# Performance work log

Measured on AMD Instinct MI355X. Metric: run time of the kernel, lower is better.

Reference implementation:

```python
import jax, jax.numpy as jnp
from jax import lax
import numpy as np

B, N, C = 128, 196, 768
H = 8
HD = C // H  # 96
FF = 3       # focusing factor
KS = 5       # dwc kernel size


def setup_inputs() -> dict:
    key = jax.random.key(0)
    ks = jax.random.split(key, 12)
    std = 0.02
    inp = {
        'x': jax.random.normal(ks[0], (B, N, C), dtype=jnp.float32),
        'Wq': jax.random.normal(ks[1], (C, C), dtype=jnp.float32) * std,
        'bq': jnp.zeros((C,), dtype=jnp.float32),
        'Wk': jax.random.normal(ks[2], (C, C), dtype=jnp.float32) * std,
        'bk': jnp.zeros((C,), dtype=jnp.float32),
        'Wv': jax.random.normal(ks[3], (C, C), dtype=jnp.float32) * std,
        'bv': jnp.zeros((C,), dtype=jnp.float32),
        'pos_enc': jax.random.normal(ks[4], (1, N, C), dtype=jnp.float32) * std,
        'scale_param': jnp.zeros((1, 1, C), dtype=jnp.float32),
        'dwc_w': jax.random.normal(ks[5], (HD, 1, KS, KS), dtype=jnp.float32) * np.sqrt(2.0 / (KS * KS)),
        'dwc_b': jnp.zeros((HD,), dtype=jnp.float32),
        'Wp': jax.random.normal(ks[6], (C, C), dtype=jnp.float32) * std,
        'bp': jnp.zeros((C,), dtype=jnp.float32),
    }
    return inp


def _focused_attn(x, Wq, bq, Wk, bk, Wv, bv, pos_enc, scale_param, dwc_w, dwc_b, Wp, bp):
    b, n, c = x.shape
    q = x @ Wq + bq
    k = x @ Wk + bk
    v = x @ Wv + bv
    k = k + pos_enc

    scale = jax.nn.softplus(scale_param)
    q = (jax.nn.relu(q) + 1e-6) / scale
    k = (jax.nn.relu(k) + 1e-6) / scale
    # focusing: raise to power FF, restore original L2 norm (over full channel dim)
    q_norm = jnp.linalg.norm(q, axis=-1, keepdims=True)
    k_norm = jnp.linalg.norm(k, axis=-1, keepdims=True)
    q = q ** FF
    k = k ** FF
    q = q / jnp.linalg.norm(q, axis=-1, keepdims=True) * q_norm
    k = k / jnp.linalg.norm(k, axis=-1, keepdims=True) * k_norm

    # (b, n, H*hd) -> (b*H, n, hd)
    def split_heads(t):
        return t.reshape(b, n, H, HD).transpose(0, 2, 1, 3).reshape(b * H, n, HD)

    q, k, v = split_heads(q), split_heads(k), split_heads(v)

    i = j = n
    cdim = ddim = HD
    z = 1.0 / (jnp.einsum('bic,bc->bi', q, k.sum(axis=1)) + 1e-6)
    if i * j * (cdim + ddim) > cdim * ddim * (i + j):
        kv = jnp.einsum('bjc,bjd->bcd', k, v)              # (b*H, hd, hd)
        out = jnp.einsum('bic,bcd,bi->bid', q, kv, z)
    else:
        qk = jnp.einsum('bic,bjc->bij', q, k)
        out = jnp.einsum('bij,bjd,bi->bid', qk, v, z)

    # depthwise conv feature map on v reshaped to sqrt(n) x sqrt(n)
    num = int(round(n ** 0.5))
    fm = v.transpose(0, 2, 1).reshape(b * H, HD, num, num)
    fm = lax.conv_general_dilated(
        fm, dwc_w, window_strides=(1, 1), padding='SAME',
        feature_group_count=HD,
        dimension_numbers=('NCHW', 'OIHW', 'NCHW'))
    fm = fm + dwc_b[None, :, None, None]
    fm = fm.reshape(b * H, HD, n).transpose(0, 2, 1)

    out = out + fm
    out = out.reshape(b, H, n, HD).transpose(0, 2, 1, 3).reshape(b, n, c)
    return out @ Wp + bp


def reference(x, Wq, bq, Wk, bk, Wv, bv, pos_enc, scale_param, dwc_w, dwc_b, Wp, bp):
    return _focused_attn(x, Wq, bq, Wk, bk, Wv, bv, pos_enc, scale_param, dwc_w, dwc_b, Wp, bp)
```

## Files before the change

kernel.cpp:

```cpp
#include <hip/hip_runtime.h>
#include <hip/hip_bf16.h>
#include <math.h>


#define MROWS 25088
#define CDIM 768
#define HDIM 96
#define NTOK 196
#define BHN 1024
#define K2 1536
#define LDP 40

typedef __attribute__((ext_vector_type(8))) short bf16x8;
typedef __attribute__((ext_vector_type(4))) float f32x4;

__device__ __forceinline__ short f2bf(float x) {
  unsigned u = __float_as_uint(x);
  unsigned r = (u + 0x7fffu + ((u >> 16) & 1u)) >> 16;
  return (short)r;
}
__device__ __forceinline__ float bf2f(short s) {
  return __uint_as_float(((unsigned)(unsigned short)s) << 16);
}

__global__ __launch_bounds__(256) void split_wt(const float* __restrict__ W0,
                                                const float* __restrict__ W1,
                                                const float* __restrict__ W2,
                                                const float* __restrict__ W3,
                                                short* __restrict__ outbase) {
  const float* W;
  switch (blockIdx.z) {
    case 0: W = W0; break;
    case 1: W = W1; break;
    case 2: W = W2; break;
    default: W = W3; break;
  }
  short* O = outbase + (size_t)blockIdx.z * 768 * K2;
  __shared__ float t[32][33];
  const int n0 = blockIdx.x * 32, k0 = blockIdx.y * 32;
  const int tx = threadIdx.x & 31, ty = threadIdx.x >> 5;
#pragma unroll
  for (int i = 0; i < 32; i += 8) t[ty + i][tx] = W[(size_t)(k0 + ty + i) * 768 + n0 + tx];
  __syncthreads();
#pragma unroll
  for (int i = 0; i < 32; i += 8) {
    float v = t[tx][ty + i];
    short h = f2bf(v), l = f2bf(v - bf2f(h));
    O[(size_t)(n0 + ty + i) * K2 + k0 + tx] = h;
    O[(size_t)(n0 + ty + i) * K2 + 768 + k0 + tx] = l;
  }
}

__device__ __forceinline__ void gemm_mfma_body(const float* __restrict__ A,
                                               const short* __restrict__ Bt2,
                                               const float* __restrict__ bias,
                                               const float* __restrict__ pos,
                                               float* __restrict__ C, bool addPos) {
  __shared__ short Ah[128 * LDP];
  __shared__ short Al[128 * LDP];
  __shared__ short Bh[128 * LDP];
  __shared__ short Bl[128 * LDP];
  const int tid = threadIdx.x;
  const int lane = tid & 63;
  const int w = tid >> 6, wr = w >> 1, wc = w & 1;
  const int row0 = blockIdx.y * 128, col0 = blockIdx.x * 128;

  const int srow = tid >> 1;
  const int scol = (tid & 1) << 4;
  const float* gA = A + (size_t)(row0 + srow) * CDIM + scol;
  const short* gBh = Bt2 + (size_t)(col0 + srow) * K2 + scol;
  short* lAh = Ah + srow * LDP + scol;
  short* lAl = Al + srow * LDP + scol;
  short* lBh = Bh + srow * LDP + scol;
  short* lBl = Bl + srow * LDP + scol;

  f32x4 acc[4][4];
#pragma unroll
  for (int i = 0; i < 4; i++)
#pragma unroll
    for (int j = 0; j < 4; j++) acc[i][j] = (f32x4){0.f, 0.f, 0.f, 0.f};

  const int fr = lane & 15;
  const int kg = (lane >> 4) << 3;

#pragma unroll 1
  for (int k0 = 0; k0 < CDIM; k0 += 32) {
    float av[16];
    *(float4*)&av[0]  = *(const float4*)(gA + k0);
    *(float4*)&av[4]  = *(const float4*)(gA + k0 + 4);
    *(float4*)&av[8]  = *(const float4*)(gA + k0 + 8);
    *(float4*)&av[12] = *(const float4*)(gA + k0 + 12);
    bf16x8 bh0 = *(const bf16x8*)(gBh + k0);
    bf16x8 bh1 = *(const bf16x8*)(gBh + k0 + 8);
    bf16x8 bl0 = *(const bf16x8*)(gBh + 768 + k0);
    bf16x8 bl1 = *(const bf16x8*)(gBh + 768 + k0 + 8);

    bf16x8 ahv[2], alv[2];
#pragma unroll
    for (int i = 0; i < 16; i++) {
      short hh = f2bf(av[i]);
      short ll = f2bf(av[i] - bf2f(hh));
      ahv[i >> 3][i & 7] = hh;
      alv[i >> 3][i & 7] = ll;
    }

    __syncthreads();
    *(bf16x8*)(lAh) = ahv[0]; *(bf16x8*)(lAh + 8) = ahv[1];
    *(bf16x8*)(lAl) = alv[0]; *(bf16x8*)(lAl + 8) = alv[1];
    *(bf16x8*)(lBh) = bh0;    *(bf16x8*)(lBh + 8) = bh1;
    *(bf16x8*)(lBl) = bl0;    *(bf16x8*)(lBl + 8) = bl1;
    __syncthreads();

    bf16x8 fah[4], fal[4], fbh[4], fbl[4];
#pragma unroll
    for (int i = 0; i < 4; i++) {
      const int ar = (wr * 64 + i * 16 + fr) * LDP + kg;
      const int br = (wc * 64 + i * 16 + fr) * LDP + kg;
      fah[i] = *(const bf16x8*)&Ah[ar];
      fal[i] = *(const bf16x8*)&Al[ar];
      fbh[i] = *(const bf16x8*)&Bh[br];
      fbl[i] = *(const bf16x8*)&Bl[br];
    }
#pragma unroll
    for (int i = 0; i < 4; i++)
#pragma unroll
      for (int j = 0; j < 4; j++)
        acc[i][j] = __builtin_amdgcn_mfma_f32_16x16x32_bf16(fah[i], fbh[j], acc[i][j], 0, 0, 0);
#pragma unroll
    for (int i = 0; i < 4; i++)
#pragma unroll
      for (int j = 0; j < 4; j++)
        acc[i][j] = __builtin_amdgcn_mfma_f32_16x16x32_bf16(fah[i], fbl[j], acc[i][j], 0, 0, 0);
#pragma unroll
    for (int i = 0; i < 4; i++)
#pragma unroll
      for (int j = 0; j < 4; j++)
        acc[i][j] = __builtin_amdgcn_mfma_f32_16x16x32_bf16(fal[i], fbh[j], acc[i][j], 0, 0, 0);
  }

  const int rg = (lane >> 4) * 4;
#pragma unroll
  for (int i = 0; i < 4; i++) {
#pragma unroll
    for (int j = 0; j < 4; j++) {
      f32x4 v = acc[i][j];
      const int gcol = col0 + wc * 64 + j * 16 + fr;
      const float bb = bias[gcol];
#pragma unroll
      for (int r = 0; r < 4; r++) {
        const int grow = row0 + wr * 64 + i * 16 + rg + r;
        float val = v[r] + bb;
        if (addPos) val += pos[(grow % NTOK) * CDIM + gcol];
        C[(size_t)grow * CDIM + gcol] = val;
      }
    }
  }
}

__global__ __launch_bounds__(256) void mfma_qkv(const float* __restrict__ x,
    const short* __restrict__ wt2,
    const float* __restrict__ b0, const float* __restrict__ b1, const float* __restrict__ b2,
    const float* __restrict__ pos,
    float* __restrict__ o0, float* __restrict__ o1, float* __restrict__ o2) {
  const short* Bt; const float* bias; float* C; bool addPos = false;
  switch (blockIdx.z) {
    case 0: Bt = wt2;                        bias = b0; C = o0; break;
    case 1: Bt = wt2 + (size_t)768 * K2;     bias = b1; C = o1; addPos = true; break;
    default: Bt = wt2 + (size_t)2 * 768 * K2; bias = b2; C = o2; break;
  }
  gemm_mfma_body(x, Bt, bias, pos, C, addPos);
}

__global__ __launch_bounds__(256) void mfma_proj(const float* __restrict__ y,
    const short* __restrict__ wt2p, const float* __restrict__ bias,
    float* __restrict__ C) {
  gemm_mfma_body(y, wt2p, bias, nullptr, C, false);
}

__device__ __forceinline__ void block_reduce2(float& a, float& b, float* sbuf, int tid) {
#pragma unroll
  for (int off = 32; off > 0; off >>= 1) {
    a += __shfl_down(a, off, 64);
    b += __shfl_down(b, off, 64);
  }
  __syncthreads();
  if ((tid & 63) == 0) {
    int w = tid >> 6;
    sbuf[w] = a;
    sbuf[4 + w] = b;
  }
  __syncthreads();
  a = sbuf[0] + sbuf[1] + sbuf[2] + sbuf[3];
  b = sbuf[4] + sbuf[5] + sbuf[6] + sbuf[7];
}

__global__ __launch_bounds__(256) void focus_kernel(float* __restrict__ q,
                                                    float* __restrict__ k,
                                                    const float* __restrict__ sp) {
  const int row = blockIdx.x;
  const int tid = threadIdx.x;
  __shared__ float sbuf[8];
  float* qb = q + (size_t)row * CDIM;
  float* kb = k + (size_t)row * CDIM;

  float tq[3], tk[3];
  float sq = 0.f, sk = 0.f;
#pragma unroll
  for (int s = 0; s < 3; s++) {
    int c = tid + s * 256;
    float scp = sp[c];
    float scale = fmaxf(scp, 0.f) + log1pf(expf(-fabsf(scp)));
    float aq = (fmaxf(qb[c], 0.f) + 1e-6f) / scale;
    float ak = (fmaxf(kb[c], 0.f) + 1e-6f) / scale;
    tq[s] = aq; tk[s] = ak;
    sq += aq * aq; sk += ak * ak;
  }
  block_reduce2(sq, sk, sbuf, tid);
  float nq1 = sqrtf(sq), nk1 = sqrtf(sk);

  float uq[3], uk[3];
  float s2q = 0.f, s2k = 0.f;
#pragma unroll
  for (int s = 0; s < 3; s++) {
    uq[s] = tq[s] * tq[s] * tq[s];
    uk[s] = tk[s] * tk[s] * tk[s];
    s2q += uq[s] * uq[s];
    s2k += uk[s] * uk[s];
  }
  block_reduce2(s2q, s2k, sbuf, tid);
  float rq = nq1 / sqrtf(s2q);
  float rk = nk1 / sqrtf(s2k);
#pragma unroll
  for (int s = 0; s < 3; s++) {
    int c = tid + s * 256;
    qb[c] = uq[s] * rq;
    kb[c] = uk[s] * rk;
  }
}

__global__ __launch_bounds__(128) void ksum_kernel(const float* __restrict__ k,
                                                   float* __restrict__ ksum) {
  const int bh = blockIdx.x;
  const int b = bh >> 3, h = bh & 7;
  const int d = threadIdx.x;
  if (d >= HDIM) return;
  const float* base = k + (size_t)(b * NTOK) * CDIM + h * HDIM + d;
  float s = 0.f;
  for (int j = 0; j < NTOK; ++j) s += base[(size_t)j * CDIM];
  ksum[bh * HDIM + d] = s;
}

__global__ __launch_bounds__(256) void kv_kernel(const float* __restrict__ k,
                                                 const float* __restrict__ v,
                                                 float* __restrict__ kv) {
  const int bh = blockIdx.x;
  const int b = bh >> 3, h = bh & 7;
  const size_t base = (size_t)(b * NTOK) * CDIM + h * HDIM;
  __shared__ float ks[28][96];
  __shared__ float vs[28][96];
  const int tid = threadIdx.x;
  const int tx = tid & 15, ty = tid >> 4;
  float acc[6][6];
#pragma unroll
  for (int i = 0; i < 6; i++)
#pragma unroll
    for (int j = 0; j < 6; j++) acc[i][j] = 0.f;

  for (int j0 = 0; j0 < NTOK; j0 += 28) {
    for (int idx = tid; idx < 28 * 96; idx += 256) {
      int jr = idx / 96, d = idx % 96;
      size_t g = base + (size_t)(j0 + jr) * CDIM + d;
      ks[jr][d] = k[g];
      vs[jr][d] = v[g];
    }
    __syncthreads();
#pragma unroll 4
    for (int j = 0; j < 28; ++j) {
      float a[6], bb[6];
#pragma unroll
      for (int i = 0; i < 6; i++) a[i] = ks[j][ty * 6 + i];
#pragma unroll
      for (int i = 0; i < 6; i++) bb[i] = vs[j][tx * 6 + i];
#pragma unroll
      for (int i = 0; i < 6; i++)
#pragma unroll
        for (int jj = 0; jj < 6; jj++) acc[i][jj] += a[i] * bb[jj];
    }
    __syncthreads();
  }
#pragma unroll
  for (int i = 0; i < 6; i++)
#pragma unroll
    for (int j = 0; j < 6; j++)
      kv[(size_t)bh * (HDIM * HDIM) + (ty * 6 + i) * HDIM + tx * 6 + j] = acc[i][j];
}

__global__ __launch_bounds__(256) void attn_out_kernel(const float* __restrict__ q,
                                                       const float* __restrict__ kvmat,
                                                       const float* __restrict__ ksum,
                                                       float* __restrict__ y) {
  const int bh = blockIdx.x;
  const int b = bh >> 3, h = bh & 7;
  const size_t base = (size_t)(b * NTOK) * CDIM + h * HDIM;
  __shared__ float kvs[HDIM * HDIM];
  __shared__ float qs[64][97];
  __shared__ float ksum_s[HDIM];
  const int tid = threadIdx.x;
  const int tx = tid & 15, ty = tid >> 4;
  const int d0 = tx * 6;

  for (int idx = tid; idx < HDIM * HDIM; idx += 256) kvs[idx] = kvmat[(size_t)bh * (HDIM * HDIM) + idx];
  if (tid < HDIM) ksum_s[tid] = ksum[bh * HDIM + tid];

  for (int i0 = 0; i0 < NTOK; i0 += 64) {
    int nrows = NTOK - i0; if (nrows > 64) nrows = 64;
    __syncthreads();
    for (int idx = tid; idx < nrows * 96; idx += 256) {
      int rr = idx / 96, d = idx % 96;
      qs[rr][d] = q[base + (size_t)(i0 + rr) * CDIM + d];
    }
    __syncthreads();

    float zz[4];
#pragma unroll
    for (int rr = 0; rr < 4; rr++) {
      int r = ty * 4 + rr;
      float part = 0.f;
#pragma unroll
      for (int i = 0; i < 6; i++) part += qs[r][d0 + i] * ksum_s[d0 + i];
#pragma unroll
      for (int m = 8; m >= 1; m >>= 1) part += __shfl_xor(part, m, 16);
      zz[rr] = 1.f / (part + 1e-6f);
    }

    float acc[4][6];
#pragma unroll
    for (int rr = 0; rr < 4; rr++)
#pragma unroll
      for (int i = 0; i < 6; i++) acc[rr][i] = 0.f;

    for (int c = 0; c < HDIM; ++c) {
      float kvv[6];
#pragma unroll
      for (int i = 0; i < 6; i++) kvv[i] = kvs[c * HDIM + d0 + i];
#pragma unroll
      for (int rr = 0; rr < 4; rr++) {
        float qv = qs[ty * 4 + rr][c];
#pragma unroll
        for (int i = 0; i < 6; i++) acc[rr][i] += qv * kvv[i];
      }
    }
#pragma unroll
    for (int rr = 0; rr < 4; rr++) {
      int r = i0 + ty * 4 + rr;
      if (r < NTOK) {
#pragma unroll
        for (int i = 0; i < 6; i++) y[base + (size_t)r * CDIM + d0 + i] = acc[rr][i] * zz[rr];
      }
    }
  }
}

__global__ __launch_bounds__(256) void dwconv_kernel(const float* __restrict__ v,
                                                     const float* __restrict__ w,
                                                     const float* __restrict__ bias,
                                                     float* __restrict__ y) {
  const int bh = blockIdx.x;
  const int b = bh >> 3, h = bh & 7;
  const int ch0 = blockIdx.y * 32;
  const size_t base = (size_t)(b * NTOK) * CDIM + h * HDIM + ch0;
  __shared__ float vs[NTOK][32];
  __shared__ float ws_s[32][25];
  const int tid = threadIdx.x;

  for (int idx = tid; idx < NTOK * 32; idx += 256) {
    int j = idx >> 5, ch = idx & 31;
    vs[j][ch] = v[base + (size_t)j * CDIM + ch];
  }
  for (int idx = tid; idx < 32 * 25; idx += 256) {
    int ch = idx / 25, kk = idx % 25;
    ws_s[ch][kk] = w[(ch0 + ch) * 25 + kk];
  }
  __syncthreads();

  const int ch = tid & 31, pg = tid >> 5;
  const float bval = bias[ch0 + ch];
  for (int p = pg; p < NTOK; p += 8) {
    int r = p / 14, cl = p % 14;
    float acc = 0.f;
#pragma unroll
    for (int dr = 0; dr < 5; dr++) {
      int rr = r + dr - 2;
      if (rr < 0 || rr >= 14) continue;
#pragma unroll
      for (int dc = 0; dc < 5; dc++) {
        int cc = cl + dc - 2;
        if (cc < 0 || cc >= 14) continue;
        acc += vs[rr * 14 + cc][ch] * ws_s[ch][dr * 5 + dc];
      }
    }
    y[base + (size_t)p * CDIM + ch] += acc + bval;
  }
}

extern "C" void kernel_launch(void* const* d_in, const int* in_sizes, int n_in,
                              void* d_out, int out_size, void* d_ws, size_t ws_size,
                              hipStream_t stream) {
  const float* x    = (const float*)d_in[0];
  const float* Wq   = (const float*)d_in[1];
  const float* bq   = (const float*)d_in[2];
  const float* Wk   = (const float*)d_in[3];
  const float* bk   = (const float*)d_in[4];
  const float* Wv   = (const float*)d_in[5];
  const float* bv   = (const float*)d_in[6];
  const float* pos  = (const float*)d_in[7];
  const float* sp   = (const float*)d_in[8];
  const float* dwcw = (const float*)d_in[9];
  const float* dwcb = (const float*)d_in[10];
  const float* Wp   = (const float*)d_in[11];
  const float* bp   = (const float*)d_in[12];
  float* out = (float*)d_out;

  const size_t MC = (size_t)MROWS * CDIM;
  char* ws = (char*)d_ws;
  float* k    = (float*)(ws);
  float* v    = (float*)(ws + MC * 4);
  short* wt2  = (short*)(ws + 2 * MC * 4);
  float* kv   = (float*)(ws + 2 * MC * 4 + (size_t)4 * 768 * K2 * 2);
  float* ksum = kv + (size_t)BHN * HDIM * HDIM;
  float* q = out;
  float* y = k;

  split_wt<<<dim3(24, 24, 4), 256, 0, stream>>>(Wq, Wk, Wv, Wp, wt2);
  mfma_qkv<<<dim3(6, 196, 3), 256, 0, stream>>>(x, wt2, bq, bk, bv, pos, q, k, v);
  focus_kernel<<<MROWS, 256, 0, stream>>>(q, k, sp);
  ksum_kernel<<<BHN, 128, 0, stream>>>(k, ksum);
  kv_kernel<<<BHN, 256, 0, stream>>>(k, v, kv);
  attn_out_kernel<<<BHN, 256, 0, stream>>>(q, kv, ksum, y);
  dwconv_kernel<<<dim3(BHN, 3), 256, 0, stream>>>(v, dwcw, dwcb, y);
  mfma_proj<<<dim3(6, 196, 1), 256, 0, stream>>>(y, wt2 + (size_t)3 * 768 * K2, bp, out);
}
```

Before: 1.010 ms.

## Use direct global-to-LDS loads with swizzle, tile remap, and wave-per-row focus

The GEMM body now loads the pre-split bf16 weight tiles straight into LDS with global_load_lds. It replaces the padded LDS layout with an XOR-swizzled unpadded one to avoid bank conflicts, remaps block indices for locality, and uses packed bf16x2 conversion for the activation hi/lo split. The focus kernel now processes one row per wavefront with float4 accesses and shuffle-only reductions, which removes block-level syncs and quarters the launch count. These changes aim to cut LDS traffic, register pressure and sync overhead, but the swizzle and tile remap must exactly match the fragment reads.

```diff
diff --git a/kernel.cpp b/kernel.cpp
--- a/kernel.cpp
+++ b/kernel.cpp
@@ -9,7 +9,6 @@
 #define NTOK 196
 #define BHN 1024
 #define K2 1536
-#define LDP 40
 
 typedef __attribute__((ext_vector_type(8))) short bf16x8;
 typedef __attribute__((ext_vector_type(4))) float f32x4;
@@ -21,6 +20,27 @@
 }
 __device__ __forceinline__ float bf2f(short s) {
   return __uint_as_float(((unsigned)(unsigned short)s) << 16);
+}
+
+__device__ __forceinline__ void gload16(const short* g, short* l) {
+  __builtin_amdgcn_global_load_lds(
+      (const __attribute__((address_space(1))) void*)g,
+      (__attribute__((address_space(3))) void*)l, 16, 0, 0);
+}
+
+__device__ __forceinline__ unsigned cvt2(float x, float y, float& rx, float& ry) {
+  __hip_bfloat162 hb = __float22bfloat162_rn(make_float2(x, y));
+  float2 hf = __bfloat1622float2(hb);
+  rx = x - hf.x; ry = y - hf.y;
+  unsigned u;
+  __builtin_memcpy(&u, &hb, 4);
+  return u;
+}
+__device__ __forceinline__ unsigned cvt2n(float x, float y) {
+  __hip_bfloat162 hb = __float22bfloat162_rn(make_float2(x, y));
+  unsigned u;
+  __builtin_memcpy(&u, &hb, 4);
+  return u;
 }
 
 __global__ __launch_bounds__(256) void split_wt(const float* __restrict__ W0,
@@ -56,23 +76,37 @@
                                                const float* __restrict__ bias,
                                                const float* __restrict__ pos,
                                                float* __restrict__ C, bool addPos) {
-  __shared__ short Ah[128 * LDP];
-  __shared__ short Al[128 * LDP];
-  __shared__ short Bh[128 * LDP];
-  __shared__ short Bl[128 * LDP];
+  __shared__ short Ah[128 * 32];
+  __shared__ short Al[128 * 32];
+  __shared__ short Bh[128 * 32];
+  __shared__ short Bl[128 * 32];
   const int tid = threadIdx.x;
   const int lane = tid & 63;
   const int w = tid >> 6, wr = w >> 1, wc = w & 1;
-  const int row0 = blockIdx.y * 128, col0 = blockIdx.x * 128;
-
-  const int srow = tid >> 1;
-  const int scol = (tid & 1) << 4;
-  const float* gA = A + (size_t)(row0 + srow) * CDIM + scol;
-  const short* gBh = Bt2 + (size_t)(col0 + srow) * K2 + scol;
-  short* lAh = Ah + srow * LDP + scol;
-  short* lAl = Al + srow * LDP + scol;
-  short* lBh = Bh + srow * LDP + scol;
-  short* lBl = Bl + srow * LDP + scol;
+
+  const int hw = blockIdx.x + 6 * blockIdx.y;
+  const int tile = (hw & 7) * 147 + (hw >> 3);
+  const int bx = tile % 6, by = tile / 6;
+  const int row0 = by * 128, col0 = bx * 128;
+
+  const int ar = tid >> 1;
+  const int ah_ = tid & 1;
+  const int am = (tid >> 2) & 3;
+  const int s0 = (2 * ah_) ^ am, s1 = (2 * ah_ + 1) ^ am;
+  const float* gA = A + (size_t)(row0 + ar) * CDIM + ah_ * 16;
+  short* lAh0 = Ah + ar * 32 + s0 * 8;
+  short* lAh1 = Ah + ar * 32 + s1 * 8;
+  short* lAl0 = Al + ar * 32 + s0 * 8;
+  short* lAl1 = Al + ar * 32 + s1 * 8;
+
+  const int brow = w * 32 + (lane >> 2);
+  const int bslot = (lane & 3) ^ ((lane >> 3) & 3);
+  const short* gBh = Bt2 + (size_t)(col0 + brow) * K2 + bslot * 8;
+  const short* gBl = gBh + 768;
+  short* ldsBh0 = Bh + (w * 32) * 32;
+  short* ldsBh1 = Bh + (w * 32 + 16) * 32;
+  short* ldsBl0 = Bl + (w * 32) * 32;
+  short* ldsBl1 = Bl + (w * 32 + 16) * 32;
 
   f32x4 acc[4][4];
 #pragma unroll
@@ -81,45 +115,50 @@
     for (int j = 0; j < 4; j++) acc[i][j] = (f32x4){0.f, 0.f, 0.f, 0.f};
 
   const int fr = lane & 15;
-  const int kg = (lane >> 4) << 3;
+  const int k16 = lane >> 4;
+  const int rslot = k16 ^ ((fr >> 1) & 3);
+  const int rofs = fr * 32 + rslot * 8;
 
 #pragma unroll 1
   for (int k0 = 0; k0 < CDIM; k0 += 32) {
-    float av[16];
-    *(float4*)&av[0]  = *(const float4*)(gA + k0);
-    *(float4*)&av[4]  = *(const float4*)(gA + k0 + 4);
-    *(float4*)&av[8]  = *(const float4*)(gA + k0 + 8);
-    *(float4*)&av[12] = *(const float4*)(gA + k0 + 12);
-    bf16x8 bh0 = *(const bf16x8*)(gBh + k0);
-    bf16x8 bh1 = *(const bf16x8*)(gBh + k0 + 8);
-    bf16x8 bl0 = *(const bf16x8*)(gBh + 768 + k0);
-    bf16x8 bl1 = *(const bf16x8*)(gBh + 768 + k0 + 8);
-
-    bf16x8 ahv[2], alv[2];
-#pragma unroll
-    for (int i = 0; i < 16; i++) {
-      short hh = f2bf(av[i]);
-      short ll = f2bf(av[i] - bf2f(hh));
-      ahv[i >> 3][i & 7] = hh;
-      alv[i >> 3][i & 7] = ll;
-    }
-
-    __syncthreads();
-    *(bf16x8*)(lAh) = ahv[0]; *(bf16x8*)(lAh + 8) = ahv[1];
-    *(bf16x8*)(lAl) = alv[0]; *(bf16x8*)(lAl + 8) = alv[1];
-    *(bf16x8*)(lBh) = bh0;    *(bf16x8*)(lBh + 8) = bh1;
-    *(bf16x8*)(lBl) = bl0;    *(bf16x8*)(lBl + 8) = bl1;
+    float4 a0 = *(const float4*)(gA + k0);
+    float4 a1 = *(const float4*)(gA + k0 + 4);
+    float4 a2 = *(const float4*)(gA + k0 + 8);
+    float4 a3 = *(const float4*)(gA + k0 + 12);
+    float r[16];
+    unsigned h0 = cvt2(a0.x, a0.y, r[0], r[1]);
+    unsigned h1 = cvt2(a0.z, a0.w, r[2], r[3]);
+    unsigned h2 = cvt2(a1.x, a1.y, r[4], r[5]);
+    unsigned h3 = cvt2(a1.z, a1.w, r[6], r[7]);
+    unsigned h4 = cvt2(a2.x, a2.y, r[8], r[9]);
+    unsigned h5 = cvt2(a2.z, a2.w, r[10], r[11]);
+    unsigned h6 = cvt2(a3.x, a3.y, r[12], r[13]);
+    unsigned h7 = cvt2(a3.z, a3.w, r[14], r[15]);
+    unsigned l0 = cvt2n(r[0], r[1]),  l1 = cvt2n(r[2], r[3]);
+    unsigned l2 = cvt2n(r[4], r[5]),  l3 = cvt2n(r[6], r[7]);
+    unsigned l4 = cvt2n(r[8], r[9]),  l5 = cvt2n(r[10], r[11]);
+    unsigned l6 = cvt2n(r[12], r[13]), l7 = cvt2n(r[14], r[15]);
+
+    __syncthreads();
+    gload16(gBh + k0, ldsBh0);
+    gload16(gBh + 16 * K2 + k0, ldsBh1);
+    gload16(gBl + k0, ldsBl0);
+    gload16(gBl + 16 * K2 + k0, ldsBl1);
+    *(uint4*)lAh0 = make_uint4(h0, h1, h2, h3);
+    *(uint4*)lAh1 = make_uint4(h4, h5, h6, h7);
+    *(uint4*)lAl0 = make_uint4(l0, l1, l2, l3);
+    *(uint4*)lAl1 = make_uint4(l4, l5, l6, l7);
     __syncthreads();
 
     bf16x8 fah[4], fal[4], fbh[4], fbl[4];
 #pragma unroll
     for (int i = 0; i < 4; i++) {
-      const int ar = (wr * 64 + i * 16 + fr) * LDP + kg;
-      const int br = (wc * 64 + i * 16 + fr) * LDP + kg;
-      fah[i] = *(const bf16x8*)&Ah[ar];
-      fal[i] = *(const bf16x8*)&Al[ar];
-      fbh[i] = *(const bf16x8*)&Bh[br];
-      fbl[i] = *(const bf16x8*)&Bl[br];
+      const int arr = (wr * 64 + i * 16) * 32 + rofs;
+      const int brr = (wc * 64 + i * 16) * 32 + rofs;
+      fah[i] = *(const bf16x8*)&Ah[arr];
+      fal[i] = *(const bf16x8*)&Al[arr];
+      fbh[i] = *(const bf16x8*)&Bh[brr];
+      fbl[i] = *(const bf16x8*)&Bl[brr];
     }
 #pragma unroll
     for (int i = 0; i < 4; i++)
@@ -147,9 +186,9 @@
       const int gcol = col0 + wc * 64 + j * 16 + fr;
       const float bb = bias[gcol];
 #pragma unroll
-      for (int r = 0; r < 4; r++) {
-        const int grow = row0 + wr * 64 + i * 16 + rg + r;
-        float val = v[r] + bb;
+      for (int r2 = 0; r2 < 4; r2++) {
+        const int grow = row0 + wr * 64 + i * 16 + rg + r2;
+        float val = v[r2] + bb;
         if (addPos) val += pos[(grow % NTOK) * CDIM + gcol];
         C[(size_t)grow * CDIM + gcol] = val;
       }
@@ -164,8 +203,8 @@
     float* __restrict__ o0, float* __restrict__ o1, float* __restrict__ o2) {
   const short* Bt; const float* bias; float* C; bool addPos = false;
   switch (blockIdx.z) {
-    case 0: Bt = wt2;                        bias = b0; C = o0; break;
-    case 1: Bt = wt2 + (size_t)768 * K2;     bias = b1; C = o1; addPos = true; break;
+    case 0: Bt = wt2;                         bias = b0; C = o0; break;
+    case 1: Bt = wt2 + (size_t)768 * K2;      bias = b1; C = o1; addPos = true; break;
     default: Bt = wt2 + (size_t)2 * 768 * K2; bias = b2; C = o2; break;
   }
   gemm_mfma_body(x, Bt, bias, pos, C, addPos);
@@ -177,64 +216,72 @@
   gemm_mfma_body(y, wt2p, bias, nullptr, C, false);
 }
 
-__device__ __forceinline__ void block_reduce2(float& a, float& b, float* sbuf, int tid) {
+__device__ __forceinline__ void wave_reduce2(float& a, float& b) {
 #pragma unroll
   for (int off = 32; off > 0; off >>= 1) {
-    a += __shfl_down(a, off, 64);
-    b += __shfl_down(b, off, 64);
-  }
-  __syncthreads();
-  if ((tid & 63) == 0) {
-    int w = tid >> 6;
-    sbuf[w] = a;
-    sbuf[4 + w] = b;
-  }
-  __syncthreads();
-  a = sbuf[0] + sbuf[1] + sbuf[2] + sbuf[3];
-  b = sbuf[4] + sbuf[5] + sbuf[6] + sbuf[7];
+    a += __shfl_xor(a, off, 64);
+    b += __shfl_xor(b, off, 64);
+  }
 }
 
 __global__ __launch_bounds__(256) void focus_kernel(float* __restrict__ q,
                                                     float* __restrict__ k,
                                                     const float* __restrict__ sp) {
-  const int row = blockIdx.x;
-  const int tid = threadIdx.x;
-  __shared__ float sbuf[8];
+  const int row = blockIdx.x * 4 + (threadIdx.x >> 6);
+  const int lane = threadIdx.x & 63;
   float* qb = q + (size_t)row * CDIM;
   float* kb = k + (size_t)row * CDIM;
 
-  float tq[3], tk[3];
+  float tq[12], tk[12];
   float sq = 0.f, sk = 0.f;
 #pragma unroll
   for (int s = 0; s < 3; s++) {
-    int c = tid + s * 256;
-    float scp = sp[c];
-    float scale = fmaxf(scp, 0.f) + log1pf(expf(-fabsf(scp)));
-    float aq = (fmaxf(qb[c], 0.f) + 1e-6f) / scale;
-    float ak = (fmaxf(kb[c], 0.f) + 1e-6f) / scale;
-    tq[s] = aq; tk[s] = ak;
-    sq += aq * aq; sk += ak * ak;
-  }
-  block_reduce2(sq, sk, sbuf, tid);
-  float nq1 = sqrtf(sq), nk1 = sqrtf(sk);
-
-  float uq[3], uk[3];
+    const int c = s * 256 + lane * 4;
+    float4 qv = *(const float4*)&qb[c];
+    float4 kv4 = *(const float4*)&kb[c];
+    float4 spv = *(const float4*)&sp[c];
+#pragma unroll
+    for (int j = 0; j < 4; j++) {
+      float scp = j == 0 ? spv.x : j == 1 ? spv.y : j == 2 ? spv.z : spv.w;
+      float qq  = j == 0 ? qv.x  : j == 1 ? qv.y  : j == 2 ? qv.z  : qv.w;
+      float kk  = j == 0 ? kv4.x : j == 1 ? kv4.y : j == 2 ? kv4.z : kv4.w;
+      float scale = fmaxf(scp, 0.f) + log1pf(expf(-fabsf(scp)));
+      float inv = 1.f / scale;
+      float aq = (fmaxf(qq, 0.f) + 1e-6f) * inv;
+      float ak = (fmaxf(kk, 0.f) + 1e-6f) * inv;
+      tq[s * 4 + j] = aq; tk[s * 4 + j] = ak;
+      sq += aq * aq; sk += ak * ak;
+    }
+  }
+  wave_reduce2(sq, sk);
+  const float nq1 = sqrtf(sq), nk1 = sqrtf(sk);
+
   float s2q = 0.f, s2k = 0.f;
 #pragma unroll
+  for (int j = 0; j < 12; j++) {
+    float cq = tq[j] * tq[j] * tq[j];
+    float ck = tk[j] * tk[j] * tk[j];
+    s2q += cq * cq; s2k += ck * ck;
+  }
+  wave_reduce2(s2q, s2k);
+  const float rq = nq1 / sqrtf(s2q);
+  const float rk = nk1 / sqrtf(s2k);
+
+#pragma unroll
   for (int s = 0; s < 3; s++) {
-    uq[s] = tq[s] * tq[s] * tq[s];
-    uk[s] = tk[s] * tk[s] * tk[s];
-    s2q += uq[s] * uq[s];
-    s2k += uk[s] * uk[s];
-  }
-  block_reduce2(s2q, s2k, sbuf, tid);
-  float rq = nq1 / sqrtf(s2q);
-  float rk = nk1 / sqrtf(s2k);
-#pragma unroll
-  for (int s = 0; s < 3; s++) {
-    int c = tid + s * 256;
-    qb[c] = uq[s] * rq;
-    kb[c] = uk[s] * rk;
+    const int c = s * 256 + lane * 4;
+    float4 oq, ok;
+#pragma unroll
+    for (int j = 0; j < 4; j++) {
+      float a = tq[s * 4 + j], b = tk[s * 4 + j];
+      float vq = a * a * a * rq, vk = b * b * b * rk;
+      if (j == 0) { oq.x = vq; ok.x = vk; }
+      else if (j == 1) { oq.y = vq; ok.y = vk; }
+      else if (j == 2) { oq.z = vq; ok.z = vk; }
+      else { oq.w = vq; ok.w = vk; }
+    }
+    *(float4*)&qb[c] = oq;
+    *(float4*)&kb[c] = ok;
   }
 }
 
@@ -324,10 +371,10 @@
     float zz[4];
 #pragma unroll
     for (int rr = 0; rr < 4; rr++) {
-      int r = ty * 4 + rr;
+      int r2 = ty * 4 + rr;
       float part = 0.f;
 #pragma unroll
-      for (int i = 0; i < 6; i++) part += qs[r][d0 + i] * ksum_s[d0 + i];
+      for (int i = 0; i < 6; i++) part += qs[r2][d0 + i] * ksum_s[d0 + i];
 #pragma unroll
       for (int m = 8; m >= 1; m >>= 1) part += __shfl_xor(part, m, 16);
       zz[rr] = 1.f / (part + 1e-6f);
@@ -352,10 +399,10 @@
     }
 #pragma unroll
     for (int rr = 0; rr < 4; rr++) {
-      int r = i0 + ty * 4 + rr;
-      if (r < NTOK) {
-#pragma unroll
-        for (int i = 0; i < 6; i++) y[base + (size_t)r * CDIM + d0 + i] = acc[rr][i] * zz[rr];
+      int r2 = i0 + ty * 4 + rr;
+      if (r2 < NTOK) {
+#pragma unroll
+        for (int i = 0; i < 6; i++) y[base + (size_t)r2 * CDIM + d0 + i] = acc[rr][i] * zz[rr];
       }
     }
   }
@@ -386,11 +433,11 @@
   const int ch = tid & 31, pg = tid >> 5;
   const float bval = bias[ch0 + ch];
   for (int p = pg; p < NTOK; p += 8) {
-    int r = p / 14, cl = p % 14;
+    int r2 = p / 14, cl = p % 14;
     float acc = 0.f;
 #pragma unroll
     for (int dr = 0; dr < 5; dr++) {
-      int rr = r + dr - 2;
+      int rr = r2 + dr - 2;
       if (rr < 0 || rr >= 14) continue;
 #pragma unroll
       for (int dc = 0; dc < 5; dc++) {
@@ -433,7 +480,7 @@
 
   split_wt<<<dim3(24, 24, 4), 256, 0, stream>>>(Wq, Wk, Wv, Wp, wt2);
   mfma_qkv<<<dim3(6, 196, 3), 256, 0, stream>>>(x, wt2, bq, bk, bv, pos, q, k, v);
-  focus_kernel<<<MROWS, 256, 0, stream>>>(q, k, sp);
+  focus_kernel<<<MROWS / 4, 256, 0, stream>>>(q, k, sp);
   ksum_kernel<<<BHN, 128, 0, stream>>>(k, ksum);
   kv_kernel<<<BHN, 256, 0, stream>>>(k, v, kv);
   attn_out_kernel<<<BHN, 256, 0, stream>>>(q, kv, ksum, y);
```

Result: faster. 937.6 us (-7.2%).
